# Kernel tuning notes

Measured on AMD Instinct MI355X. Metric: run time of the kernel, lower is better.

## Reference

```python
import jax, jax.numpy as jnp
import numpy as np

B, S = 4096, 8192

def setup_inputs() -> dict:
    key = jax.random.key(0)
    c = jax.random.normal(key, (B, S), dtype=jnp.float32)
    beta = jnp.asarray(10.0, dtype=jnp.float32)
    return {"c": c, "beta": beta}

def reference(c, beta):
    # Original per-step recurrence:
    #   delta_i = (1/beta) * logsumexp([beta*delta_{i-1}, beta*(c_i + delta_{i-1})])
    #           = delta_{i-1} + (1/beta) * log(1 + exp(beta * c_i))
    # i.e. an exact prefix sum of softplus(beta*c)/beta along S.
    # (Note: the torch code stacks delta_prev, not 0, as the first branch,
    #  so the logsumexp telescopes to a cumulative sum.)
    step = jax.nn.softplus(beta * c) / beta          # (B, S)
    return jnp.cumsum(step, axis=1)                  # (B, S) propagated delays
```

## Files before the change

### kernel.cpp

```cpp
#include <hip/hip_runtime.h>
#include <hip/hip_bf16.h>


#define ROW_S   8192
#define BLOCK_T 256
#define NJ      (ROW_S / 4 / BLOCK_T)
#define NWAVE   (BLOCK_T / 64)

__device__ __forceinline__ float softplus_step(float c, float beta, float inv_beta) {
    float tb = beta * c;
    float a  = fabsf(tb);
    float e  = __expf(-a);
    float l  = __logf(1.0f + e);
    return (fmaxf(tb, 0.0f) + l) * inv_beta;
}

__global__ __launch_bounds__(BLOCK_T) void softplus_cumsum_kernel(
    const float* __restrict__ c,
    const float* __restrict__ beta_p,
    float* __restrict__ out)
{
    __shared__ float wave_sums[NJ][NWAVE];

    const int t    = threadIdx.x;
    const int lane = t & 63;
    const int wave = t >> 6;
    const size_t row_base = (size_t)blockIdx.x * ROW_S;

    const float beta     = beta_p[0];
    const float inv_beta = 1.0f / beta;

    const float4* __restrict__ in4  = (const float4*)(c + row_base);
    float4*       __restrict__ out4 = (float4*)(out + row_base);

    float4 v[NJ];
    #pragma unroll
    for (int j = 0; j < NJ; ++j)
        v[j] = in4[j * BLOCK_T + t];

    float4 r[NJ];
    float  s[NJ];
    #pragma unroll
    for (int j = 0; j < NJ; ++j) {
        float a = softplus_step(v[j].x, beta, inv_beta);
        float b = softplus_step(v[j].y, beta, inv_beta);
        float d = softplus_step(v[j].z, beta, inv_beta);
        float e = softplus_step(v[j].w, beta, inv_beta);
        r[j].x = a;
        r[j].y = a + b;
        r[j].z = r[j].y + d;
        r[j].w = r[j].z + e;
        s[j]   = r[j].w;
    }

    float xscan[NJ];
    #pragma unroll
    for (int j = 0; j < NJ; ++j) {
        float x = s[j];
        #pragma unroll
        for (int d = 1; d < 64; d <<= 1) {
            float y = __shfl_up(x, d, 64);
            if (lane >= d) x += y;
        }
        xscan[j] = x;
        if (lane == 63) wave_sums[j][wave] = x;
    }
    __syncthreads();

    float carry = 0.0f;
    #pragma unroll
    for (int j = 0; j < NJ; ++j) {
        float woff = 0.0f, btot = 0.0f;
        #pragma unroll
        for (int w = 0; w < NWAVE; ++w) {
            float ws = wave_sums[j][w];
            if (w < wave) woff += ws;
            btot += ws;
        }
        const float off = carry + woff + (xscan[j] - s[j]);
        carry += btot;

        float4 o;
        o.x = r[j].x + off;
        o.y = r[j].y + off;
        o.z = r[j].z + off;
        o.w = r[j].w + off;
        out4[j * BLOCK_T + t] = o;
    }
}

extern "C" void kernel_launch(void* const* d_in, const int* in_sizes, int n_in,
                              void* d_out, int out_size, void* d_ws, size_t ws_size,
                              hipStream_t stream) {
    const float* c      = (const float*)d_in[0];
    const float* beta_p = (const float*)d_in[1];
    float*       out    = (float*)d_out;

    const int B = in_sizes[0] / ROW_S;
    softplus_cumsum_kernel<<<dim3(B), dim3(BLOCK_T), 0, stream>>>(c, beta_p, out);
}
```

Measured before the change: 232.2 us.

## Process multiple rows per block with prefetch of next row and nontemporal stores

Each block now handles up to four rows in a grid-stride pattern. It prefetches the next row's input into registers while the current row is scanned, and double-buffers the shared wave sums so rows can overlap. Block size doubles to 512 threads, and outputs use nontemporal stores to avoid polluting the cache. The aim is to hide global load latency behind compute and to cut per-block launch overhead, at the cost of higher register pressure and fewer blocks in the grid.

```diff
diff --git a/kernel.cpp b/kernel.cpp
--- a/kernel.cpp
+++ b/kernel.cpp
@@ -1,11 +1,13 @@
 #include <hip/hip_runtime.h>
-#include <hip/hip_bf16.h>
 
 
 #define ROW_S   8192
-#define BLOCK_T 256
+#define BLOCK_T 512
 #define NJ      (ROW_S / 4 / BLOCK_T)
 #define NWAVE   (BLOCK_T / 64)
+#define ROWS    4
+
+typedef float f32x4 __attribute__((ext_vector_type(4)));
 
 __device__ __forceinline__ float softplus_step(float c, float beta, float inv_beta) {
     float tb = beta * c;
@@ -15,77 +17,93 @@
     return (fmaxf(tb, 0.0f) + l) * inv_beta;
 }
 
-__global__ __launch_bounds__(BLOCK_T) void softplus_cumsum_kernel(
+__global__ __launch_bounds__(BLOCK_T, 8) void softplus_cumsum_kernel(
     const float* __restrict__ c,
     const float* __restrict__ beta_p,
-    float* __restrict__ out)
+    float* __restrict__ out,
+    int nrows, int grid)
 {
-    __shared__ float wave_sums[NJ][NWAVE];
+    __shared__ float wave_sums[2][NJ][NWAVE];
 
     const int t    = threadIdx.x;
     const int lane = t & 63;
     const int wave = t >> 6;
-    const size_t row_base = (size_t)blockIdx.x * ROW_S;
 
     const float beta     = beta_p[0];
     const float inv_beta = 1.0f / beta;
 
-    const float4* __restrict__ in4  = (const float4*)(c + row_base);
-    float4*       __restrict__ out4 = (float4*)(out + row_base);
+    const int    row0 = blockIdx.x;
+    const size_t rs4  = (size_t)grid * (ROW_S / 4);
 
-    float4 v[NJ];
+    const f32x4* __restrict__ in4  = (const f32x4*)c   + (size_t)row0 * (ROW_S / 4);
+    f32x4*       __restrict__ out4 = (f32x4*)out       + (size_t)row0 * (ROW_S / 4);
+
+    f32x4 v[NJ];
     #pragma unroll
     for (int j = 0; j < NJ; ++j)
         v[j] = in4[j * BLOCK_T + t];
 
-    float4 r[NJ];
-    float  s[NJ];
     #pragma unroll
-    for (int j = 0; j < NJ; ++j) {
-        float a = softplus_step(v[j].x, beta, inv_beta);
-        float b = softplus_step(v[j].y, beta, inv_beta);
-        float d = softplus_step(v[j].z, beta, inv_beta);
-        float e = softplus_step(v[j].w, beta, inv_beta);
-        r[j].x = a;
-        r[j].y = a + b;
-        r[j].z = r[j].y + d;
-        r[j].w = r[j].z + e;
-        s[j]   = r[j].w;
-    }
+    for (int i = 0; i < ROWS; ++i) {
+        const int cur_row = row0 + i * grid;
+        if (cur_row >= nrows) break;
 
-    float xscan[NJ];
-    #pragma unroll
-    for (int j = 0; j < NJ; ++j) {
-        float x = s[j];
+        f32x4 r[NJ];
         #pragma unroll
-        for (int d = 1; d < 64; d <<= 1) {
-            float y = __shfl_up(x, d, 64);
-            if (lane >= d) x += y;
+        for (int j = 0; j < NJ; ++j) {
+            float a = softplus_step(v[j].x, beta, inv_beta);
+            float b = softplus_step(v[j].y, beta, inv_beta);
+            float d = softplus_step(v[j].z, beta, inv_beta);
+            float e = softplus_step(v[j].w, beta, inv_beta);
+            r[j].x = a;
+            r[j].y = a + b;
+            r[j].z = r[j].y + d;
+            r[j].w = r[j].z + e;
         }
-        xscan[j] = x;
-        if (lane == 63) wave_sums[j][wave] = x;
-    }
-    __syncthreads();
 
-    float carry = 0.0f;
-    #pragma unroll
-    for (int j = 0; j < NJ; ++j) {
-        float woff = 0.0f, btot = 0.0f;
+        if (i + 1 < ROWS && cur_row + grid < nrows) {
+            #pragma unroll
+            for (int j = 0; j < NJ; ++j)
+                v[j] = in4[rs4 + j * BLOCK_T + t];
+        }
+
+        float xscan[NJ];
         #pragma unroll
-        for (int w = 0; w < NWAVE; ++w) {
-            float ws = wave_sums[j][w];
-            if (w < wave) woff += ws;
-            btot += ws;
+        for (int j = 0; j < NJ; ++j) {
+            float x = r[j].w;
+            #pragma unroll
+            for (int d = 1; d < 64; d <<= 1) {
+                float y = __shfl_up(x, d, 64);
+                if (lane >= d) x += y;
+            }
+            xscan[j] = x;
+            if (lane == 63) wave_sums[i & 1][j][wave] = x;
         }
-        const float off = carry + woff + (xscan[j] - s[j]);
-        carry += btot;
+        __syncthreads();
 
-        float4 o;
-        o.x = r[j].x + off;
-        o.y = r[j].y + off;
-        o.z = r[j].z + off;
-        o.w = r[j].w + off;
-        out4[j * BLOCK_T + t] = o;
+        float carry = 0.0f;
+        #pragma unroll
+        for (int j = 0; j < NJ; ++j) {
+            float woff = 0.0f, btot = 0.0f;
+            #pragma unroll
+            for (int w = 0; w < NWAVE; ++w) {
+                float ws = wave_sums[i & 1][j][w];
+                if (w < wave) woff += ws;
+                btot += ws;
+            }
+            const float off = carry + woff + (xscan[j] - r[j].w);
+            carry += btot;
+
+            f32x4 o;
+            o.x = r[j].x + off;
+            o.y = r[j].y + off;
+            o.z = r[j].z + off;
+            o.w = r[j].w + off;
+            __builtin_nontemporal_store(o, &out4[j * BLOCK_T + t]);
+        }
+
+        in4  += rs4;
+        out4 += rs4;
     }
 }
 
@@ -96,6 +114,9 @@
     const float* beta_p = (const float*)d_in[1];
     float*       out    = (float*)d_out;
 
-    const int B = in_sizes[0] / ROW_S;
-    softplus_cumsum_kernel<<<dim3(B), dim3(BLOCK_T), 0, stream>>>(c, beta_p, out);
+    const int B    = in_sizes[0] / ROW_S;
+    const int grid = (B + ROWS - 1) / ROWS;
+
+    softplus_cumsum_kernel<<<dim3(grid), dim3(BLOCK_T), 0, stream>>>(
+        c, beta_p, out, B, grid);
 }
```

Result: slower. 237.5 us (+2.3%).

## Assign one row per wavefront with double-buffered multi-pass prefetch scan

Applied to the files above, without the earlier changes.

The kernel moves from one block per row with a shared-memory cross-wave scan to one wavefront per row. Each wave walks its row in 8 passes of 1024 elements and keeps a running carry. Loads are double-buffered so the next-but-one pass is fetched while the current pass is scanned, which removes __syncthreads and LDS traffic. In exchange there is less memory parallelism per row and a longer serial dependency chain per wave, so throughput now depends on occupancy across the 1024 blocks.

```diff
diff --git a/kernel.cpp b/kernel.cpp
--- a/kernel.cpp
+++ b/kernel.cpp
@@ -1,11 +1,14 @@
 #include <hip/hip_runtime.h>
-#include <hip/hip_bf16.h>
 
 
 #define ROW_S   8192
-#define BLOCK_T 256
-#define NJ      (ROW_S / 4 / BLOCK_T)
-#define NWAVE   (BLOCK_T / 64)
+#define NJ      4
+#define PASS_F4 (64 * NJ)
+#define NPASS   (ROW_S / (PASS_F4 * 4))
+#define WPB     4
+#define BLOCK_T (WPB * 64)
+
+typedef float f32x4 __attribute__((ext_vector_type(4)));
 
 __device__ __forceinline__ float softplus_step(float c, float beta, float inv_beta) {
     float tb = beta * c;
@@ -15,78 +18,85 @@
     return (fmaxf(tb, 0.0f) + l) * inv_beta;
 }
 
-__global__ __launch_bounds__(BLOCK_T) void softplus_cumsum_kernel(
+__global__ __launch_bounds__(BLOCK_T, 4) void softplus_cumsum_kernel(
     const float* __restrict__ c,
     const float* __restrict__ beta_p,
-    float* __restrict__ out)
+    float* __restrict__ out,
+    int nrows)
 {
-    __shared__ float wave_sums[NJ][NWAVE];
-
-    const int t    = threadIdx.x;
-    const int lane = t & 63;
-    const int wave = t >> 6;
-    const size_t row_base = (size_t)blockIdx.x * ROW_S;
+    const int lane = threadIdx.x & 63;
+    const int wave = threadIdx.x >> 6;
+    const int row  = blockIdx.x * WPB + wave;
+    if (row >= nrows) return;
 
     const float beta     = beta_p[0];
     const float inv_beta = 1.0f / beta;
 
-    const float4* __restrict__ in4  = (const float4*)(c + row_base);
-    float4*       __restrict__ out4 = (float4*)(out + row_base);
-
-    float4 v[NJ];
-    #pragma unroll
-    for (int j = 0; j < NJ; ++j)
-        v[j] = in4[j * BLOCK_T + t];
-
-    float4 r[NJ];
-    float  s[NJ];
-    #pragma unroll
-    for (int j = 0; j < NJ; ++j) {
-        float a = softplus_step(v[j].x, beta, inv_beta);
-        float b = softplus_step(v[j].y, beta, inv_beta);
-        float d = softplus_step(v[j].z, beta, inv_beta);
-        float e = softplus_step(v[j].w, beta, inv_beta);
-        r[j].x = a;
-        r[j].y = a + b;
-        r[j].z = r[j].y + d;
-        r[j].w = r[j].z + e;
-        s[j]   = r[j].w;
-    }
-
-    float xscan[NJ];
-    #pragma unroll
-    for (int j = 0; j < NJ; ++j) {
-        float x = s[j];
-        #pragma unroll
-        for (int d = 1; d < 64; d <<= 1) {
-            float y = __shfl_up(x, d, 64);
-            if (lane >= d) x += y;
-        }
-        xscan[j] = x;
-        if (lane == 63) wave_sums[j][wave] = x;
-    }
-    __syncthreads();
+    const f32x4* __restrict__ in4  = (const f32x4*)c   + (size_t)row * (ROW_S / 4);
+    f32x4*       __restrict__ out4 = (f32x4*)out       + (size_t)row * (ROW_S / 4);
 
     float carry = 0.0f;
+
+    f32x4 va[NJ], vb[NJ];
     #pragma unroll
-    for (int j = 0; j < NJ; ++j) {
-        float woff = 0.0f, btot = 0.0f;
+    for (int j = 0; j < NJ; ++j) va[j] = in4[0 * PASS_F4 + j * 64 + lane];
+    #pragma unroll
+    for (int j = 0; j < NJ; ++j) vb[j] = in4[1 * PASS_F4 + j * 64 + lane];
+
+    auto body = [&](f32x4 (&cur)[NJ], const int p) {
+        f32x4 r[NJ];
+        float s[NJ];
         #pragma unroll
-        for (int w = 0; w < NWAVE; ++w) {
-            float ws = wave_sums[j][w];
-            if (w < wave) woff += ws;
-            btot += ws;
+        for (int j = 0; j < NJ; ++j) {
+            float a = softplus_step(cur[j].x, beta, inv_beta);
+            float b = softplus_step(cur[j].y, beta, inv_beta);
+            float d = softplus_step(cur[j].z, beta, inv_beta);
+            float e = softplus_step(cur[j].w, beta, inv_beta);
+            r[j].x = a;
+            r[j].y = a + b;
+            r[j].z = r[j].y + d;
+            r[j].w = r[j].z + e;
+            s[j]   = r[j].w;
         }
-        const float off = carry + woff + (xscan[j] - s[j]);
-        carry += btot;
 
-        float4 o;
-        o.x = r[j].x + off;
-        o.y = r[j].y + off;
-        o.z = r[j].z + off;
-        o.w = r[j].w + off;
-        out4[j * BLOCK_T + t] = o;
-    }
+        if (p + 2 < NPASS) {
+            #pragma unroll
+            for (int j = 0; j < NJ; ++j)
+                cur[j] = in4[(p + 2) * PASS_F4 + j * 64 + lane];
+        }
+
+        float xs[NJ], G[NJ];
+        #pragma unroll
+        for (int j = 0; j < NJ; ++j) {
+            float x = s[j];
+            #pragma unroll
+            for (int d = 1; d < 64; d <<= 1) {
+                float y = __shfl_up(x, d, 64);
+                if (lane >= d) x += y;
+            }
+            xs[j] = x;
+            G[j]  = __shfl(x, 63, 64);
+        }
+
+        float pre = carry;
+        #pragma unroll
+        for (int j = 0; j < NJ; ++j) {
+            const float off = pre + (xs[j] - s[j]);
+            pre += G[j];
+            f32x4 o;
+            o.x = r[j].x + off;
+            o.y = r[j].y + off;
+            o.z = r[j].z + off;
+            o.w = r[j].w + off;
+            out4[p * PASS_F4 + j * 64 + lane] = o;
+        }
+        carry = pre;
+    };
+
+    body(va, 0); body(vb, 1);
+    body(va, 2); body(vb, 3);
+    body(va, 4); body(vb, 5);
+    body(va, 6); body(vb, 7);
 }
 
 extern "C" void kernel_launch(void* const* d_in, const int* in_sizes, int n_in,
@@ -96,6 +106,9 @@
     const float* beta_p = (const float*)d_in[1];
     float*       out    = (float*)d_out;
 
-    const int B = in_sizes[0] / ROW_S;
-    softplus_cumsum_kernel<<<dim3(B), dim3(BLOCK_T), 0, stream>>>(c, beta_p, out);
+    const int B    = in_sizes[0] / ROW_S;
+    const int grid = (B + WPB - 1) / WPB;
+
+    softplus_cumsum_kernel<<<dim3(grid), dim3(BLOCK_T), 0, stream>>>(
+        c, beta_p, out, B);
 }
```

New measurement: 240.6 us. +3.6%, slower.
